# Performance work log

Measured on AMD Instinct MI355X. Metric: run time of the kernel, lower is better.

## Reference

```python
import jax, jax.numpy as jnp
import numpy as np

N_PRED, N_DRIFT, N_DW, N_NODES = 12, 2, 3, 4096
B = 128
L = N_PRED + 2 * N_DRIFT  # 16


def setup_inputs() -> dict:
    key = jax.random.key(0)
    ks = jax.random.split(key, 8)
    inp = jax.random.normal(ks[0], (B, N_NODES, N_DW, L), jnp.float32)
    ctrl = jax.random.normal(ks[1], (B, N_NODES, N_PRED), jnp.float32)
    # learned offsets (init zeros in torch; randomized here so interpolation is non-trivial)
    offset_t = jax.random.normal(ks[2], (N_DW, N_PRED), jnp.float32) * 0.5
    offset_n = jax.random.normal(ks[3], (N_DW, N_PRED), jnp.float32) * 0.5
    conv_t_w = jax.random.normal(ks[4], (1, N_DW, 3), jnp.float32) / np.sqrt(N_DW * 3)
    conv_t_b = jnp.zeros((1,), jnp.float32)
    conv_n_w = jax.random.normal(ks[5], (N_PRED, N_PRED, N_DW), jnp.float32) / np.sqrt(N_PRED * N_DW)
    conv_n_b = jnp.zeros((N_PRED,), jnp.float32)
    W = jax.random.normal(ks[6], (N_PRED, N_PRED), jnp.float32)
    bparam = jax.random.normal(ks[7], (N_NODES, N_PRED), jnp.float32)
    return dict(inp=inp, ctrl=ctrl, offset_t=offset_t, offset_n=offset_n,
                conv_t_w=conv_t_w, conv_t_b=conv_t_b, conv_n_w=conv_n_w,
                conv_n_b=conv_n_b, W=W, bparam=bparam)


def _deform(x, offset):
    # x: [BN, n_d_w, L]; offset: [n_d_w, n_pred]
    pos_add = (jnp.arange(N_PRED, dtype=jnp.float32) + N_DRIFT)[None, :]  # [1, n_pred]
    pos = jnp.tanh(offset) * N_DRIFT + pos_add                           # [d, p], in [j, j+2*drift)
    key_f = jnp.floor(pos)            # torch int(pos); pos >= 0 so floor == trunc
    frac = pos - key_f                # gradient flows to offset only through frac
    idx = key_f.astype(jnp.int32)     # [d, p]
    rows = jnp.arange(N_DW)[:, None]  # [d, 1]
    v0 = x[:, rows, idx]              # [BN, d, p]
    v1 = x[:, rows, idx + 1]
    return v0 * (1.0 - frac) + v1 * frac


def reference(inp, ctrl, offset_t, offset_n, conv_t_w, conv_t_b, conv_n_w, conv_n_b, W, bparam):
    b, n = inp.shape[0], inp.shape[1]
    x = inp.reshape(b * n, N_DW, L)
    # the written slice [n_drift:-n_drift] is exactly the interpolated region
    dt = _deform(x, offset_t)  # [BN, n_d_w, n_pred]
    dn = _deform(x, offset_n)  # [BN, n_d_w, n_pred]
    # temporal branch: Conv1d(n_d_w -> 1, k=3, pad=1)
    pred_t = jax.lax.conv_general_dilated(
        dt, conv_t_w, window_strides=(1,), padding=[(1, 1)],
        dimension_numbers=('NCH', 'OIH', 'NCH'))
    pred_t = (pred_t + conv_t_b[None, :, None]).reshape(b, n, N_PRED)
    # node branch: Conv1d(n_pred -> n_pred, k=n_d_w) over permuted [BN, n_pred, n_d_w]
    # == full contraction: out[b,o] = sum_{c,k} w[o,c,k] * dn[b,k,c]
    pred_n = (jnp.einsum('bkc,ock->bo', dn, conv_n_w) + conv_n_b).reshape(b, n, N_PRED)
    gate = jax.nn.sigmoid(jnp.einsum('bnp,pq->bnq', ctrl, W) + bparam)
    return pred_n * gate + pred_t * (1.0 - gate)
```

## Files before the change

kernel.cpp:

```cpp
#include <hip/hip_runtime.h>
#include <math.h>

#define N_PRED  12
#define N_DRIFT 2
#define N_DW    3
#define N_NODES 4096
#define BB      128
#define LL      16
#define BN      (BB * N_NODES)
#define TPB     128
#define NBLK    (BN / TPB)
#define XROW    13

__global__ void deform_precompute(const float* __restrict__ offset_t,
                                  const float* __restrict__ offset_n,
                                  const float* __restrict__ conv_t_w,
                                  const float* __restrict__ conv_n_w,
                                  float* __restrict__ Mt,
                                  float* __restrict__ Mn) {
    int t = threadIdx.x;
    if (t >= N_PRED * N_DW * LL) return;
    int q  = t % N_PRED;
    int kl = t / N_PRED;
    int k  = kl / LL;
    int l  = kl % LL;

    auto coef = [&](const float* off, int c) -> float {
        float pos = tanhf(off[k * N_PRED + c]) * (float)N_DRIFT
                    + (float)(c + N_DRIFT);
        float idf = floorf(pos);
        float fr  = pos - idf;
        int   id  = (int)idf;
        if (l == id)     return 1.0f - fr;
        if (l == id + 1) return fr;
        return 0.0f;
    };

    float mt = 0.0f;
    #pragma unroll
    for (int h = 0; h < 3; ++h) {
        int c = q - 1 + h;
        if (c < 0 || c >= N_PRED) continue;
        mt += conv_t_w[k * 3 + h] * coef(offset_t, c);
    }

    float mn = 0.0f;
    #pragma unroll
    for (int c = 0; c < N_PRED; ++c) {
        mn += conv_n_w[q * (N_PRED * N_DW) + c * N_DW + k] * coef(offset_n, c);
    }

    Mt[kl * N_PRED + q] = mt;
    Mn[kl * N_PRED + q] = mn;
}

__global__ __launch_bounds__(TPB) void deform_main(
        const float* __restrict__ inp,
        const float* __restrict__ ctrl,
        const float* __restrict__ W,
        const float* __restrict__ bparam,
        const float* __restrict__ conv_t_b,
        const float* __restrict__ conv_n_b,
        const float* __restrict__ Mt,
        const float* __restrict__ Mn,
        float* __restrict__ out) {
    __shared__ float4 xs4[TPB * XROW];
    __shared__ float4 cs4[TPB * 3];

    const int t   = threadIdx.x;
    const int tid = blockIdx.x * TPB + t;
    const int n   = tid & (N_NODES - 1);

    const float4* gin = (const float4*)inp + (size_t)blockIdx.x * (TPB * 12);
    #pragma unroll
    for (int i = 0; i < 12; ++i) {
        int A = i * TPB + t;
        float4 v = gin[A];
        xs4[(A / 12) * XROW + (A % 12)] = v;
    }
    const float4* gct = (const float4*)ctrl + (size_t)blockIdx.x * (TPB * 3);
    #pragma unroll
    for (int i = 0; i < 3; ++i) {
        int A = i * TPB + t;
        cs4[A] = gct[A];
    }
    __syncthreads();

    float x[48];
    #pragma unroll
    for (int c = 0; c < 12; ++c) {
        float4 v = xs4[t * XROW + c];
        x[4 * c + 0] = v.x; x[4 * c + 1] = v.y;
        x[4 * c + 2] = v.z; x[4 * c + 3] = v.w;
    }
    float cr[12];
    #pragma unroll
    for (int i = 0; i < 3; ++i) {
        float4 v = cs4[t * 3 + i];
        cr[4 * i + 0] = v.x; cr[4 * i + 1] = v.y;
        cr[4 * i + 2] = v.z; cr[4 * i + 3] = v.w;
    }

    float accg[12];
    {
        const float* bp = bparam + (size_t)n * N_PRED;
        #pragma unroll
        for (int i = 0; i < 3; ++i) {
            float4 v = *(const float4*)(bp + 4 * i);
            accg[4 * i + 0] = v.x; accg[4 * i + 1] = v.y;
            accg[4 * i + 2] = v.z; accg[4 * i + 3] = v.w;
        }
    }

    float acct[12], accn[12];
    float ctb = conv_t_b[0];
    #pragma unroll
    for (int q = 0; q < N_PRED; ++q) {
        acct[q] = ctb;
        accn[q] = conv_n_b[q];
    }

    #pragma unroll
    for (int kl = 0; kl < 48; ++kl) {
        float xv = x[kl];
        #pragma unroll
        for (int q = 0; q < N_PRED; ++q) {
            acct[q] = fmaf(Mt[kl * N_PRED + q], xv, acct[q]);
            accn[q] = fmaf(Mn[kl * N_PRED + q], xv, accn[q]);
        }
    }

    #pragma unroll
    for (int p = 0; p < N_PRED; ++p) {
        float cv = cr[p];
        #pragma unroll
        for (int q = 0; q < N_PRED; ++q) {
            accg[q] = fmaf(cv, W[p * N_PRED + q], accg[q]);
        }
    }

    float4 o4[3];
    float* ov = (float*)o4;
    #pragma unroll
    for (int q = 0; q < N_PRED; ++q) {
        float g = 1.0f / (1.0f + __expf(-accg[q]));
        ov[q] = accn[q] * g + acct[q] * (1.0f - g);
    }

    __syncthreads();
    #pragma unroll
    for (int j = 0; j < 3; ++j) {
        xs4[t * 3 + j] = o4[j];
    }
    __syncthreads();
    float4* gout = (float4*)out + (size_t)blockIdx.x * (TPB * 3);
    #pragma unroll
    for (int j = 0; j < 3; ++j) {
        int A = j * TPB + t;
        gout[A] = xs4[A];
    }
}

extern "C" void kernel_launch(void* const* d_in, const int* in_sizes, int n_in,
                              void* d_out, int out_size, void* d_ws, size_t ws_size,
                              hipStream_t stream) {
    const float* inp      = (const float*)d_in[0];
    const float* ctrl     = (const float*)d_in[1];
    const float* offset_t = (const float*)d_in[2];
    const float* offset_n = (const float*)d_in[3];
    const float* conv_t_w = (const float*)d_in[4];
    const float* conv_t_b = (const float*)d_in[5];
    const float* conv_n_w = (const float*)d_in[6];
    const float* conv_n_b = (const float*)d_in[7];
    const float* W        = (const float*)d_in[8];
    const float* bparam   = (const float*)d_in[9];
    float* out = (float*)d_out;

    float* Mt = (float*)d_ws;
    float* Mn = Mt + N_DW * LL * N_PRED;

    deform_precompute<<<1, 576, 0, stream>>>(offset_t, offset_n,
                                             conv_t_w, conv_n_w, Mt, Mn);
    deform_main<<<NBLK, TPB, 0, stream>>>(inp, ctrl, W, bparam,
                                          conv_t_b, conv_n_b, Mt, Mn, out);
}
```

Baseline: 203.0 us.

## Process multiple chunks per block with register prefetch of next input tile

Each block now loops over four 128-row chunks and prefetches the next chunk's input into registers while computing the current one, so global load latency overlaps compute. The ctrl and output tiles no longer go through shared memory: ctrl is loaded and the output stored directly per thread as strided float4 accesses, which are less coalesced. The grid shrinks fourfold and the prefetch buffer adds register pressure, which may lower occupancy on a memory-bound kernel.

```diff
diff --git a/kernel.cpp b/kernel.cpp
--- a/kernel.cpp
+++ b/kernel.cpp
@@ -9,7 +9,9 @@
 #define LL      16
 #define BN      (BB * N_NODES)
 #define TPB     128
-#define NBLK    (BN / TPB)
+#define CPB     4
+#define NCHUNK  (BN / TPB)
+#define NBLK    (NCHUNK / CPB)
 #define XROW    13
 
 __global__ void deform_precompute(const float* __restrict__ offset_t,
@@ -65,99 +67,100 @@
         const float* __restrict__ Mn,
         float* __restrict__ out) {
     __shared__ float4 xs4[TPB * XROW];
-    __shared__ float4 cs4[TPB * 3];
 
-    const int t   = threadIdx.x;
-    const int tid = blockIdx.x * TPB + t;
-    const int n   = tid & (N_NODES - 1);
+    const int t      = threadIdx.x;
+    const int chunk0 = blockIdx.x * CPB;
 
-    const float4* gin = (const float4*)inp + (size_t)blockIdx.x * (TPB * 12);
-    #pragma unroll
-    for (int i = 0; i < 12; ++i) {
-        int A = i * TPB + t;
-        float4 v = gin[A];
-        xs4[(A / 12) * XROW + (A % 12)] = v;
-    }
-    const float4* gct = (const float4*)ctrl + (size_t)blockIdx.x * (TPB * 3);
-    #pragma unroll
-    for (int i = 0; i < 3; ++i) {
-        int A = i * TPB + t;
-        cs4[A] = gct[A];
-    }
-    __syncthreads();
+    const float4* gin_base = (const float4*)inp;
 
-    float x[48];
-    #pragma unroll
-    for (int c = 0; c < 12; ++c) {
-        float4 v = xs4[t * XROW + c];
-        x[4 * c + 0] = v.x; x[4 * c + 1] = v.y;
-        x[4 * c + 2] = v.z; x[4 * c + 3] = v.w;
-    }
-    float cr[12];
-    #pragma unroll
-    for (int i = 0; i < 3; ++i) {
-        float4 v = cs4[t * 3 + i];
-        cr[4 * i + 0] = v.x; cr[4 * i + 1] = v.y;
-        cr[4 * i + 2] = v.z; cr[4 * i + 3] = v.w;
+    float4 pre[12];
+    {
+        const float4* gin = gin_base + (size_t)chunk0 * (TPB * 12);
+        #pragma unroll
+        for (int i = 0; i < 12; ++i) pre[i] = gin[i * TPB + t];
     }
 
-    float accg[12];
-    {
-        const float* bp = bparam + (size_t)n * N_PRED;
+    const float ctb = conv_t_b[0];
+
+    #pragma unroll 1
+    for (int k = 0; k < CPB; ++k) {
+        const int chunk = chunk0 + k;
+
         #pragma unroll
-        for (int i = 0; i < 3; ++i) {
-            float4 v = *(const float4*)(bp + 4 * i);
-            accg[4 * i + 0] = v.x; accg[4 * i + 1] = v.y;
-            accg[4 * i + 2] = v.z; accg[4 * i + 3] = v.w;
+        for (int i = 0; i < 12; ++i) {
+            int A = i * TPB + t;
+            xs4[(A / 12) * XROW + (A % 12)] = pre[i];
         }
-    }
+        __syncthreads();
 
-    float acct[12], accn[12];
-    float ctb = conv_t_b[0];
-    #pragma unroll
-    for (int q = 0; q < N_PRED; ++q) {
-        acct[q] = ctb;
-        accn[q] = conv_n_b[q];
-    }
+        if (k + 1 < CPB) {
+            const float4* gin = gin_base + (size_t)(chunk + 1) * (TPB * 12);
+            #pragma unroll
+            for (int i = 0; i < 12; ++i) pre[i] = gin[i * TPB + t];
+        }
 
-    #pragma unroll
-    for (int kl = 0; kl < 48; ++kl) {
-        float xv = x[kl];
+        const int tid = chunk * TPB + t;
+        const int n   = tid & (N_NODES - 1);
+
+        float4 cv[3], bv[3];
+        {
+            const float4* gct = (const float4*)ctrl + (size_t)tid * 3;
+            #pragma unroll
+            for (int i = 0; i < 3; ++i) cv[i] = gct[i];
+            const float4* gbp = (const float4*)bparam + (size_t)n * 3;
+            #pragma unroll
+            for (int i = 0; i < 3; ++i) bv[i] = gbp[i];
+        }
+
+        float acct[12], accn[12];
         #pragma unroll
         for (int q = 0; q < N_PRED; ++q) {
-            acct[q] = fmaf(Mt[kl * N_PRED + q], xv, acct[q]);
-            accn[q] = fmaf(Mn[kl * N_PRED + q], xv, accn[q]);
+            acct[q] = ctb;
+            accn[q] = conv_n_b[q];
         }
-    }
 
-    #pragma unroll
-    for (int p = 0; p < N_PRED; ++p) {
-        float cv = cr[p];
+        #pragma unroll
+        for (int c = 0; c < 12; ++c) {
+            float4 v = xs4[t * XROW + c];
+            #pragma unroll
+            for (int e = 0; e < 4; ++e) {
+                float xv = (e == 0) ? v.x : (e == 1) ? v.y : (e == 2) ? v.z : v.w;
+                const int kl = 4 * c + e;
+                #pragma unroll
+                for (int q = 0; q < N_PRED; ++q) {
+                    acct[q] = fmaf(Mt[kl * N_PRED + q], xv, acct[q]);
+                    accn[q] = fmaf(Mn[kl * N_PRED + q], xv, accn[q]);
+                }
+            }
+        }
+
+        float accg[12];
+        const float* bvf = (const float*)bv;
+        const float* cvf = (const float*)cv;
+        #pragma unroll
+        for (int q = 0; q < N_PRED; ++q) accg[q] = bvf[q];
+        #pragma unroll
+        for (int p = 0; p < N_PRED; ++p) {
+            float c = cvf[p];
+            #pragma unroll
+            for (int q = 0; q < N_PRED; ++q) {
+                accg[q] = fmaf(c, W[p * N_PRED + q], accg[q]);
+            }
+        }
+
+        float4 o4[3];
+        float* ov = (float*)o4;
         #pragma unroll
         for (int q = 0; q < N_PRED; ++q) {
-            accg[q] = fmaf(cv, W[p * N_PRED + q], accg[q]);
+            float g = 1.0f / (1.0f + __expf(-accg[q]));
+            ov[q] = accn[q] * g + acct[q] * (1.0f - g);
         }
-    }
 
-    float4 o4[3];
-    float* ov = (float*)o4;
-    #pragma unroll
-    for (int q = 0; q < N_PRED; ++q) {
-        float g = 1.0f / (1.0f + __expf(-accg[q]));
-        ov[q] = accn[q] * g + acct[q] * (1.0f - g);
-    }
+        float4* gout = (float4*)out + (size_t)tid * 3;
+        #pragma unroll
+        for (int j = 0; j < 3; ++j) gout[j] = o4[j];
 
-    __syncthreads();
-    #pragma unroll
-    for (int j = 0; j < 3; ++j) {
-        xs4[t * 3 + j] = o4[j];
-    }
-    __syncthreads();
-    float4* gout = (float4*)out + (size_t)blockIdx.x * (TPB * 3);
-    #pragma unroll
-    for (int j = 0; j < 3; ++j) {
-        int A = j * TPB + t;
-        gout[A] = xs4[A];
+        __syncthreads();
     }
 }
 
```

Measured after the change: 319.7 us. +57.5%, slower.

## Persistent per-wave double-buffered pipeline with async global-to-LDS loads

Applied to the files above, without the earlier changes.

Switches the main kernel to 512 persistent blocks whose waves each process 8 chunks of 64 rows. Input and ctrl tiles are double-buffered in LDS through global_load_lds, and explicit vmcnt waits let the load of the next chunk overlap compute on the current one. Block-wide syncthreads are replaced by per-wave LDS staging. The cost is fewer waves in flight (launch bounds 1, 1024 waves), and the correctness of the hand-set vmcnt counts and the LDS read ordering is fragile.

```diff
diff --git a/kernel.cpp b/kernel.cpp
--- a/kernel.cpp
+++ b/kernel.cpp
@@ -9,8 +9,8 @@
 #define LL      16
 #define BN      (BB * N_NODES)
 #define TPB     128
-#define NBLK    (BN / TPB)
-#define XROW    13
+#define CPW     8
+#define NBLK    512
 
 __global__ void deform_precompute(const float* __restrict__ offset_t,
                                   const float* __restrict__ offset_n,
@@ -54,7 +54,14 @@
     Mn[kl * N_PRED + q] = mn;
 }
 
-__global__ __launch_bounds__(TPB) void deform_main(
+typedef const __attribute__((address_space(1))) void* gas1_t;
+typedef __attribute__((address_space(3))) void* las3_t;
+
+__device__ __forceinline__ void gll16(const void* g, void* lds) {
+    __builtin_amdgcn_global_load_lds((gas1_t)g, (las3_t)lds, 16, 0, 0);
+}
+
+__global__ __launch_bounds__(TPB, 1) void deform_main(
         const float* __restrict__ inp,
         const float* __restrict__ ctrl,
         const float* __restrict__ W,
@@ -64,100 +71,122 @@
         const float* __restrict__ Mt,
         const float* __restrict__ Mn,
         float* __restrict__ out) {
-    __shared__ float4 xs4[TPB * XROW];
-    __shared__ float4 cs4[TPB * 3];
-
-    const int t   = threadIdx.x;
-    const int tid = blockIdx.x * TPB + t;
-    const int n   = tid & (N_NODES - 1);
-
-    const float4* gin = (const float4*)inp + (size_t)blockIdx.x * (TPB * 12);
-    #pragma unroll
-    for (int i = 0; i < 12; ++i) {
-        int A = i * TPB + t;
-        float4 v = gin[A];
-        xs4[(A / 12) * XROW + (A % 12)] = v;
-    }
-    const float4* gct = (const float4*)ctrl + (size_t)blockIdx.x * (TPB * 3);
-    #pragma unroll
-    for (int i = 0; i < 3; ++i) {
-        int A = i * TPB + t;
-        cs4[A] = gct[A];
-    }
-    __syncthreads();
-
-    float x[48];
-    #pragma unroll
-    for (int c = 0; c < 12; ++c) {
-        float4 v = xs4[t * XROW + c];
-        x[4 * c + 0] = v.x; x[4 * c + 1] = v.y;
-        x[4 * c + 2] = v.z; x[4 * c + 3] = v.w;
-    }
-    float cr[12];
-    #pragma unroll
-    for (int i = 0; i < 3; ++i) {
-        float4 v = cs4[t * 3 + i];
-        cr[4 * i + 0] = v.x; cr[4 * i + 1] = v.y;
-        cr[4 * i + 2] = v.z; cr[4 * i + 3] = v.w;
-    }
-
-    float accg[12];
-    {
-        const float* bp = bparam + (size_t)n * N_PRED;
+    __shared__ float4 xs4[2][2][768];
+    __shared__ float4 cs4[2][2][192];
+    __shared__ float4 os4[2][192];
+
+    const int t  = threadIdx.x;
+    const int l  = t & 63;
+    const int w  = t >> 6;
+    const int gw = blockIdx.x * 2 + w;
+    const int cbase = gw * CPW;
+
+    const char* gx = (const char*)inp;
+    const char* gc = (const char*)ctrl;
+
+    auto STAGE = [&](int b, int c) {
+        const char* sx = gx + (size_t)c * 12288 + (size_t)l * 16;
+        #pragma unroll
+        for (int j = 0; j < 12; ++j)
+            gll16(sx + j * 1024, &xs4[b][w][j * 64]);
+        const char* sc = gc + (size_t)c * 3072 + (size_t)l * 16;
+        #pragma unroll
+        for (int j = 0; j < 3; ++j)
+            gll16(sc + j * 1024, &cs4[b][w][j * 64]);
+    };
+
+    STAGE(0, cbase);
+
+    const float ctb = conv_t_b[0];
+
+    #pragma unroll 1
+    for (int k = 0; k < CPW; ++k) {
+        const int b = k & 1;
+        const int c = cbase + k;
+
+        __builtin_amdgcn_sched_barrier(0);
+        float4 bv0, bv1, bv2;
+        {
+            const int n = ((c & 63) << 6) + l;
+            const float4* gbp = (const float4*)bparam + (size_t)n * 3;
+            bv0 = gbp[0]; bv1 = gbp[1]; bv2 = gbp[2];
+        }
+        __builtin_amdgcn_sched_barrier(0);
+        if (k + 1 < CPW) STAGE(b ^ 1, c + 1);
+        __builtin_amdgcn_sched_barrier(0);
+        if (k + 1 < CPW) asm volatile("s_waitcnt vmcnt(18)");
+        else             asm volatile("s_waitcnt vmcnt(0)");
+        __builtin_amdgcn_sched_barrier(0);
+
+        float acct[12], accn[12];
+        #pragma unroll
+        for (int q = 0; q < N_PRED; ++q) {
+            acct[q] = ctb;
+            accn[q] = conv_n_b[q];
+        }
+
+        #pragma unroll
+        for (int cc = 0; cc < 12; ++cc) {
+            float4 v = xs4[b][w][l * 12 + cc];
+            #pragma unroll
+            for (int e = 0; e < 4; ++e) {
+                float xv = (e == 0) ? v.x : (e == 1) ? v.y : (e == 2) ? v.z : v.w;
+                const int kl = 4 * cc + e;
+                #pragma unroll
+                for (int q = 0; q < N_PRED; ++q) {
+                    acct[q] = fmaf(Mt[kl * N_PRED + q], xv, acct[q]);
+                    accn[q] = fmaf(Mn[kl * N_PRED + q], xv, accn[q]);
+                }
+            }
+        }
+
+        float accg[12];
+        {
+            const float* bvf0 = (const float*)&bv0;
+            const float* bvf1 = (const float*)&bv1;
+            const float* bvf2 = (const float*)&bv2;
+            #pragma unroll
+            for (int i = 0; i < 4; ++i) {
+                accg[i]     = bvf0[i];
+                accg[4 + i] = bvf1[i];
+                accg[8 + i] = bvf2[i];
+            }
+        }
+        float cr[12];
         #pragma unroll
         for (int i = 0; i < 3; ++i) {
-            float4 v = *(const float4*)(bp + 4 * i);
-            accg[4 * i + 0] = v.x; accg[4 * i + 1] = v.y;
-            accg[4 * i + 2] = v.z; accg[4 * i + 3] = v.w;
-        }
-    }
-
-    float acct[12], accn[12];
-    float ctb = conv_t_b[0];
-    #pragma unroll
-    for (int q = 0; q < N_PRED; ++q) {
-        acct[q] = ctb;
-        accn[q] = conv_n_b[q];
-    }
-
-    #pragma unroll
-    for (int kl = 0; kl < 48; ++kl) {
-        float xv = x[kl];
+            float4 v = cs4[b][w][l * 3 + i];
+            cr[4 * i + 0] = v.x; cr[4 * i + 1] = v.y;
+            cr[4 * i + 2] = v.z; cr[4 * i + 3] = v.w;
+        }
+        #pragma unroll
+        for (int p = 0; p < N_PRED; ++p) {
+            float cv = cr[p];
+            #pragma unroll
+            for (int q = 0; q < N_PRED; ++q) {
+                accg[q] = fmaf(cv, W[p * N_PRED + q], accg[q]);
+            }
+        }
+
+        float4 o4[3];
+        float* ov = (float*)o4;
         #pragma unroll
         for (int q = 0; q < N_PRED; ++q) {
-            acct[q] = fmaf(Mt[kl * N_PRED + q], xv, acct[q]);
-            accn[q] = fmaf(Mn[kl * N_PRED + q], xv, accn[q]);
-        }
-    }
-
-    #pragma unroll
-    for (int p = 0; p < N_PRED; ++p) {
-        float cv = cr[p];
-        #pragma unroll
-        for (int q = 0; q < N_PRED; ++q) {
-            accg[q] = fmaf(cv, W[p * N_PRED + q], accg[q]);
-        }
-    }
-
-    float4 o4[3];
-    float* ov = (float*)o4;
-    #pragma unroll
-    for (int q = 0; q < N_PRED; ++q) {
-        float g = 1.0f / (1.0f + __expf(-accg[q]));
-        ov[q] = accn[q] * g + acct[q] * (1.0f - g);
-    }
-
-    __syncthreads();
-    #pragma unroll
-    for (int j = 0; j < 3; ++j) {
-        xs4[t * 3 + j] = o4[j];
-    }
-    __syncthreads();
-    float4* gout = (float4*)out + (size_t)blockIdx.x * (TPB * 3);
-    #pragma unroll
-    for (int j = 0; j < 3; ++j) {
-        int A = j * TPB + t;
-        gout[A] = xs4[A];
+            float g = 1.0f / (1.0f + __expf(-accg[q]));
+            ov[q] = accn[q] * g + acct[q] * (1.0f - g);
+        }
+
+        #pragma unroll
+        for (int j = 0; j < 3; ++j) {
+            os4[w][3 * l + j] = o4[j];
+        }
+        float4* gout = (float4*)out + (size_t)c * 192;
+        #pragma unroll
+        for (int j = 0; j < 3; ++j) {
+            int s = j * 64 + l;
+            gout[s] = os4[w][s];
+        }
+        __builtin_amdgcn_sched_barrier(0);
     }
 }
 
```

Result: slower. 207.8 us (+2.3%).
